# Kernel tuning notes

Measured on AMD Instinct MI355X. Metric: run time of the kernel, lower is better.

Reference implementation:

```python
import jax, jax.numpy as jnp
import numpy as np

B, N = 64, 8192
RW_APPROX_THRES = 0.6
L_CUTOFF = 100
EPS = 1e-12


def _skew(k):
    kx, ky, kz = k[..., 0], k[..., 1], k[..., 2]
    z = jnp.zeros_like(kx)
    return jnp.stack([
        jnp.stack([z, -kz, ky], -1),
        jnp.stack([kz, z, -kx], -1),
        jnp.stack([-ky, kx, z], -1)], -2)


def so3_exp(v):
    # v: [..., 3] rotation vector -> [..., 3, 3] rotation matrix (Rodrigues)
    theta = jnp.linalg.norm(v, axis=-1, keepdims=True)
    k = v / jnp.maximum(theta, 1e-12)
    K = _skew(k)
    s = jnp.sin(theta)[..., None]
    c = jnp.cos(theta)[..., None]
    I = jnp.eye(3, dtype=v.dtype)
    return I + s * K + (1.0 - c) * (K @ K)


def so3_log(r):
    # r: [..., 3, 3] rotation matrix -> [..., 3] rotation vector
    tr = r[..., 0, 0] + r[..., 1, 1] + r[..., 2, 2]
    cos = jnp.clip((tr - 1.0) * 0.5, -1.0 + 1e-7, 1.0 - 1e-7)
    theta = jnp.arccos(cos)  # [...]
    a = jnp.stack([
        r[..., 2, 1] - r[..., 1, 2],
        r[..., 0, 2] - r[..., 2, 0],
        r[..., 1, 0] - r[..., 0, 1]], axis=-1)  # [..., 3]
    scale = theta / (2.0 * jnp.sin(theta))
    return a * scale[..., None]


def igso3_grad_log_pdf(sigma, omega):
    # sigma: [B], omega: [B, N] angles in (0, pi)
    # f(w) = sum_l (2l+1) exp(-l(l+1) sigma^2 / 2) sin((l+1/2) w) / sin(w/2)
    l = jnp.arange(L_CUTOFF + 1, dtype=omega.dtype)          # [L]
    s2 = (sigma ** 2)[:, None, None]                          # [B,1,1]
    coef = (2.0 * l + 1.0) * jnp.exp(-l * (l + 1.0) * s2 / 2.0)  # [B,1,L]
    w = omega[..., None]                                      # [B,N,1]
    lh = l + 0.5
    sin_h = jnp.sin(w / 2.0)
    cos_h = jnp.cos(w / 2.0)
    sin_lw = jnp.sin(lh * w)                                  # [B,N,L]
    f = jnp.sum(coef * sin_lw / sin_h, axis=-1)               # [B,N]
    df = jnp.sum(coef * (lh * jnp.cos(lh * w) * sin_h - 0.5 * cos_h * sin_lw) / (sin_h ** 2), axis=-1)
    return df / (f + EPS)


def setup_inputs() -> dict:
    key = jax.random.key(0)
    k1, k2, k3, k4, k5 = jax.random.split(key, 5)
    ax1 = jax.random.normal(k1, (B, N, 3), dtype=jnp.float32)
    ax1 = ax1 / jnp.linalg.norm(ax1, axis=-1, keepdims=True)
    ang1 = jax.random.uniform(k2, (B, N, 1), minval=0.1, maxval=3.0, dtype=jnp.float32)
    r_t = so3_exp(ax1 * ang1)
    ax2 = jax.random.normal(k3, (B, N, 3), dtype=jnp.float32)
    ax2 = ax2 / jnp.linalg.norm(ax2, axis=-1, keepdims=True)
    ang2 = jax.random.uniform(k4, (B, N, 1), minval=0.1, maxval=3.0, dtype=jnp.float32)
    rh_0 = so3_exp(ax2 * ang2)
    sigma_t = jax.random.uniform(k5, (B,), minval=0.7, maxval=2.5, dtype=jnp.float32)
    return {"r_t": r_t, "rh_0": rh_0, "sigma_t": sigma_t}


def reference(r_t, rh_0, sigma_t):
    # RotationDiffuser.score with left=True
    r_z = jnp.einsum('bnij,bnkj->bnik', r_t, rh_0)  # r_t @ rh_0^T
    v_z = so3_log(r_z)                               # [B,N,3]
    rw_approx = -v_z / (sigma_t[:, None, None] ** 2)
    w = jnp.linalg.norm(v_z, axis=-1)                # [B,N]
    dlogf_dw = igso3_grad_log_pdf(sigma_t, w)        # [B,N]
    score = jnp.where(sigma_t[:, None, None] > RW_APPROX_THRES,
                      v_z * dlogf_dw[..., None] / (w[..., None] + EPS),
                      rw_approx)
    return score
```

## Files before the change

### kernel.cpp

```cpp
#include <hip/hip_runtime.h>
#include <math.h>


#define BD 256
#define LMAX 100

__device__ __forceinline__ float opq(float x) { __asm__("" : "+v"(x)); return x; }
__device__ __forceinline__ float MULF(float a, float b) { return opq(a * b); }
__device__ __forceinline__ float ADDF(float a, float b) { return opq(a + b); }
__device__ __forceinline__ float SUBF(float a, float b) { return opq(a - b); }
__device__ __forceinline__ float FMAF(float a, float b, float c) { return opq(__builtin_fmaf(a, b, c)); }
__device__ __forceinline__ float DOT3F(float a0, float b0, float a1, float b1,
                                       float a2, float b2) {
    return FMAF(a2, b2, FMAF(a1, b1, MULF(a0, b0)));
}

__device__ __forceinline__ double asin_p(double u) {
    double p = 0.00515311;
    p = __builtin_fma(p, u, 0.00574004);
    p = __builtin_fma(p, u, 0.0064472);
    p = __builtin_fma(p, u, 0.007312526);
    p = __builtin_fma(p, u, 0.008390335809616815);
    p = __builtin_fma(p, u, 0.009761609529194078);
    p = __builtin_fma(p, u, 0.011551800896139706);
    p = __builtin_fma(p, u, 0.01396484375);
    p = __builtin_fma(p, u, 0.017352764423076924);
    p = __builtin_fma(p, u, 0.022372159090909092);
    p = __builtin_fma(p, u, 0.030381944444444444);
    p = __builtin_fma(p, u, 0.044642857142857144);
    p = __builtin_fma(p, u, 0.075);
    p = __builtin_fma(p, u, 0.16666666666666666);
    p = __builtin_fma(p, u, 1.0);
    return p;
}
__device__ __forceinline__ double sin_p(double u) {
    double p = 2.8114572543455206e-15;
    p = __builtin_fma(p, u, -7.647163731819816e-13);
    p = __builtin_fma(p, u, 1.6059043836821613e-10);
    p = __builtin_fma(p, u, -2.505210838544172e-8);
    p = __builtin_fma(p, u, 2.7557319223985893e-6);
    p = __builtin_fma(p, u, -1.984126984126984e-4);
    p = __builtin_fma(p, u, 8.333333333333333e-3);
    p = __builtin_fma(p, u, -0.16666666666666666);
    p = __builtin_fma(p, u, 1.0);
    return p;
}
__device__ __forceinline__ double cos_p(double u) {
    double p = 4.779477332387385e-14;
    p = __builtin_fma(p, u, -1.1470745597729725e-11);
    p = __builtin_fma(p, u, 2.08767569878681e-9);
    p = __builtin_fma(p, u, -2.755731922398589e-7);
    p = __builtin_fma(p, u, 2.48015873015873e-5);
    p = __builtin_fma(p, u, -1.3888888888888889e-3);
    p = __builtin_fma(p, u, 0.041666666666666664);
    p = __builtin_fma(p, u, -0.5);
    p = __builtin_fma(p, u, 1.0);
    return p;
}
__device__ __forceinline__ double exp_d(double x) {
    double n = __builtin_rint(x * 1.4426950408889634);
    double r = __builtin_fma(-n, 6.93147180369123816490e-01, x);
    r = __builtin_fma(-n, 1.90821492927058770002e-10, r);
    double p = 2.08767569878681e-9;
    p = __builtin_fma(p, r, 2.505210838544172e-8);
    p = __builtin_fma(p, r, 2.755731922398589e-7);
    p = __builtin_fma(p, r, 2.48015873015873e-5);
    p = __builtin_fma(p, r, 1.984126984126984e-4);
    p = __builtin_fma(p, r, 1.3888888888888889e-3);
    p = __builtin_fma(p, r, 8.333333333333333e-3);
    p = __builtin_fma(p, r, 0.041666666666666664);
    p = __builtin_fma(p, r, 0.16666666666666666);
    p = __builtin_fma(p, r, 0.5);
    p = __builtin_fma(p, r, 1.0);
    p = __builtin_fma(p, r, 1.0);
    return p * exp2(n);
}

__global__ __launch_bounds__(BD) void rot_score_kernel(
    const float* __restrict__ rt, const float* __restrict__ rh,
    const float* __restrict__ sigma_t, float* __restrict__ out, int npts)
{
    __shared__ float  sA[BD * 9];
    __shared__ float  sB[BD * 9];
    __shared__ float  sCoef[LMAX + 1];
    __shared__ double sCoefL[LMAX + 1];

    const int tid = threadIdx.x;
    const int blocksPerB = npts / BD;
    const int b = blockIdx.x / blocksPerB;
    const size_t base = (size_t)blockIdx.x * BD;

    const float sigma = sigma_t[b];
    const float s2 = MULF(sigma, sigma);

    const float* gA = rt + base * 9;
    const float* gB = rh + base * 9;
#pragma unroll
    for (int k = 0; k < 9; ++k) {
        int i = tid + k * BD;
        sA[i] = gA[i];
        sB[i] = gB[i];
    }
    if (tid <= LMAX) {
        float lf = (float)tid;
        float t  = MULF(MULF(-lf, lf + 1.0f), s2);
        float arg = t * 0.5f;
        float e  = (float)exp_d((double)arg);
        float cf = MULF(2.0f * lf + 1.0f, e);
        sCoef[tid]  = cf;
        sCoefL[tid] = (double)cf * ((double)lf + 0.5);
    }
    __syncthreads();

    const int o = tid * 9;
    float a0 = sA[o+0], a1 = sA[o+1], a2 = sA[o+2];
    float a3 = sA[o+3], a4 = sA[o+4], a5 = sA[o+5];
    float a6 = sA[o+6], a7 = sA[o+7], a8 = sA[o+8];
    float b0 = sB[o+0], b1 = sB[o+1], b2 = sB[o+2];
    float b3 = sB[o+3], b4 = sB[o+4], b5 = sB[o+5];
    float b6 = sB[o+6], b7 = sB[o+7], b8 = sB[o+8];

    float m00 = DOT3F(a0,b0, a1,b1, a2,b2);
    float m11 = DOT3F(a3,b3, a4,b4, a5,b5);
    float m22 = DOT3F(a6,b6, a7,b7, a8,b8);
    float m01 = DOT3F(a0,b3, a1,b4, a2,b5);
    float m10 = DOT3F(a3,b0, a4,b1, a5,b2);
    float m02 = DOT3F(a0,b6, a1,b7, a2,b8);
    float m20 = DOT3F(a6,b0, a7,b1, a8,b2);
    float m12 = DOT3F(a3,b6, a4,b7, a5,b8);
    float m21 = DOT3F(a6,b3, a7,b4, a8,b5);

    float tr   = ADDF(ADDF(m00, m11), m22);
    float cosv = MULF(SUBF(tr, 1.0f), 0.5f);
    const float CLO = (float)(-1.0 + 1e-7);
    const float CHI = (float)( 1.0 - 1e-7);
    cosv = fminf(fmaxf(cosv, CLO), CHI);

    double xd = (double)cosv;
    double axd = fabs(xd);
    bool mid = (axd <= 0.5);
    double uedge = (1.0 - axd) * 0.5;
    double m = mid ? xd : sqrt(uedge);
    double asv = m * asin_p(m * m);
    double th_mid  = 1.5707963267948966 - asv;
    double th_edge = (xd > 0.0) ? (2.0 * asv)
                                : (3.141592653589793 - 2.0 * asv);
    double theta_d = mid ? th_mid : th_edge;
    float theta = (float)theta_d;

    double td = (double)theta;
    double e  = (td > 1.5707963267948966) ? (3.141592653589793 - td) : td;
    float st  = (float)(e * sin_p(e * e));

    float scale = (float)((double)theta / (double)(2.0f * st));
    float ax = SUBF(m21, m12);
    float ay = SUBF(m02, m20);
    float az = SUBF(m10, m01);
    float vx = MULF(ax, scale);
    float vy = MULF(ay, scale);
    float vz = MULF(az, scale);
    float ssum = ADDF(ADDF(MULF(vx,vx), MULF(vy,vy)), MULF(vz,vz));
    float w = (float)sqrt((double)ssum);

    double wd = (double)w;
    double h  = 0.5 * wd;
    double h2 = h * h;
    double shd = h * sin_p(h2);
    double chd = cos_p(h2);
    double swd = 2.0 * shd * chd;
    double cwd = 1.0 - 2.0 * shd * shd;

    double s = shd, c = chd;
    double S1 = 0.0, S2 = 0.0;
    for (int l = 0; l <= LMAX; ++l) {
        double cf = (double)sCoef[l];
        if (cf == 0.0) break;
        S1 = __builtin_fma(cf,        s, S1);
        S2 = __builtin_fma(sCoefL[l], c, S2);
        double ns = __builtin_fma(s, cwd,  c * swd);
        double nc = __builtin_fma(c, cwd, -(s * swd));
        s = ns; c = nc;
    }
    double f  = S1 / shd;
    double df = (S2 * shd - 0.5 * chd * S1) / (shd * shd);
    double g  = df / ((f + 1e-12) * (wd + 1e-12));

    float ox, oy, oz;
    if (sigma > 0.6f) {
        ox = (float)((double)vx * g);
        oy = (float)((double)vy * g);
        oz = (float)((double)vz * g);
    } else {
        ox = (float)((double)(-vx) / (double)s2);
        oy = (float)((double)(-vy) / (double)s2);
        oz = (float)((double)(-vz) / (double)s2);
    }

    __syncthreads();
    sA[tid * 3 + 0] = ox;
    sA[tid * 3 + 1] = oy;
    sA[tid * 3 + 2] = oz;
    __syncthreads();
    float* gO = out + base * 3;
#pragma unroll
    for (int k = 0; k < 3; ++k) {
        int i = tid + k * BD;
        gO[i] = sA[i];
    }
}

extern "C" void kernel_launch(void* const* d_in, const int* in_sizes, int n_in,
                              void* d_out, int out_size, void* d_ws, size_t ws_size,
                              hipStream_t stream) {
    const float* r_t     = (const float*)d_in[0];
    const float* rh_0    = (const float*)d_in[1];
    const float* sigma_t = (const float*)d_in[2];
    float* out = (float*)d_out;

    const int nB = in_sizes[2];
    const int n_elem = in_sizes[0] / 9;
    const int npts = n_elem / nB;
    const int grid = n_elem / BD;

    rot_score_kernel<<<grid, BD, 0, stream>>>(r_t, rh_0, sigma_t, out, npts);
}
```

Measured before the change: 84.72 us.

## Compute IGSO3 series in fp32 with sigma-based truncation and packed coefficients

Moves the l-series recurrence, the half-angle sin/cos polynomials and the final score arithmetic from double to float. The loop count is now derived analytically from sigma, replacing the per-iteration zero check. Coefficients are packed as float2 in shared memory, and exp2 is replaced by exponent bit construction. This removes the slow fp64 throughput on the dominant loop, at the risk of lower accuracy near small angles and in the f/df cancellation.

```diff
diff --git a/kernel.cpp b/kernel.cpp
--- a/kernel.cpp
+++ b/kernel.cpp
@@ -33,7 +33,7 @@
     p = __builtin_fma(p, u, 1.0);
     return p;
 }
-__device__ __forceinline__ double sin_p(double u) {
+__device__ __forceinline__ double sin_pd(double u) {
     double p = 2.8114572543455206e-15;
     p = __builtin_fma(p, u, -7.647163731819816e-13);
     p = __builtin_fma(p, u, 1.6059043836821613e-10);
@@ -45,19 +45,27 @@
     p = __builtin_fma(p, u, 1.0);
     return p;
 }
-__device__ __forceinline__ double cos_p(double u) {
-    double p = 4.779477332387385e-14;
-    p = __builtin_fma(p, u, -1.1470745597729725e-11);
-    p = __builtin_fma(p, u, 2.08767569878681e-9);
-    p = __builtin_fma(p, u, -2.755731922398589e-7);
-    p = __builtin_fma(p, u, 2.48015873015873e-5);
-    p = __builtin_fma(p, u, -1.3888888888888889e-3);
-    p = __builtin_fma(p, u, 0.041666666666666664);
-    p = __builtin_fma(p, u, -0.5);
-    p = __builtin_fma(p, u, 1.0);
+__device__ __forceinline__ float sin_pf(float u) {
+    float p = -2.5052108e-8f;
+    p = __builtin_fmaf(p, u, 2.75573192e-6f);
+    p = __builtin_fmaf(p, u, -1.98412698e-4f);
+    p = __builtin_fmaf(p, u, 8.33333333e-3f);
+    p = __builtin_fmaf(p, u, -0.166666667f);
+    p = __builtin_fmaf(p, u, 1.0f);
+    return p;
+}
+__device__ __forceinline__ float cos_pf(float u) {
+    float p = 2.08767570e-9f;
+    p = __builtin_fmaf(p, u, -2.75573192e-7f);
+    p = __builtin_fmaf(p, u, 2.48015873e-5f);
+    p = __builtin_fmaf(p, u, -1.38888889e-3f);
+    p = __builtin_fmaf(p, u, 4.16666667e-2f);
+    p = __builtin_fmaf(p, u, -0.5f);
+    p = __builtin_fmaf(p, u, 1.0f);
     return p;
 }
 __device__ __forceinline__ double exp_d(double x) {
+    if (x < -110.0) return 0.0;
     double n = __builtin_rint(x * 1.4426950408889634);
     double r = __builtin_fma(-n, 6.93147180369123816490e-01, x);
     r = __builtin_fma(-n, 1.90821492927058770002e-10, r);
@@ -73,7 +81,9 @@
     p = __builtin_fma(p, r, 0.5);
     p = __builtin_fma(p, r, 1.0);
     p = __builtin_fma(p, r, 1.0);
-    return p * exp2(n);
+    long long ni = (long long)n;
+    double p2 = __longlong_as_double((1023ll + ni) << 52);
+    return p * p2;
 }
 
 __global__ __launch_bounds__(BD) void rot_score_kernel(
@@ -82,8 +92,7 @@
 {
     __shared__ float  sA[BD * 9];
     __shared__ float  sB[BD * 9];
-    __shared__ float  sCoef[LMAX + 1];
-    __shared__ double sCoefL[LMAX + 1];
+    __shared__ float2 sC[LMAX + 1];
 
     const int tid = threadIdx.x;
     const int blocksPerB = npts / BD;
@@ -107,8 +116,7 @@
         float arg = t * 0.5f;
         float e  = (float)exp_d((double)arg);
         float cf = MULF(2.0f * lf + 1.0f, e);
-        sCoef[tid]  = cf;
-        sCoefL[tid] = (double)cf * ((double)lf + 0.5);
+        sC[tid] = make_float2(cf, cf * (lf + 0.5f));
     }
     __syncthreads();
 
@@ -150,8 +158,7 @@
 
     double td = (double)theta;
     double e  = (td > 1.5707963267948966) ? (3.141592653589793 - td) : td;
-    float st  = (float)(e * sin_p(e * e));
-
+    float st  = (float)(e * sin_pd(e * e));
     float scale = (float)((double)theta / (double)(2.0f * st));
     float ax = SUBF(m21, m12);
     float ay = SUBF(m02, m20);
@@ -162,38 +169,37 @@
     float ssum = ADDF(ADDF(MULF(vx,vx), MULF(vy,vy)), MULF(vz,vz));
     float w = (float)sqrt((double)ssum);
 
-    double wd = (double)w;
-    double h  = 0.5 * wd;
-    double h2 = h * h;
-    double shd = h * sin_p(h2);
-    double chd = cos_p(h2);
-    double swd = 2.0 * shd * chd;
-    double cwd = 1.0 - 2.0 * shd * shd;
-
-    double s = shd, c = chd;
-    double S1 = 0.0, S2 = 0.0;
-    for (int l = 0; l <= LMAX; ++l) {
-        double cf = (double)sCoef[l];
-        if (cf == 0.0) break;
-        S1 = __builtin_fma(cf,        s, S1);
-        S2 = __builtin_fma(sCoefL[l], c, S2);
-        double ns = __builtin_fma(s, cwd,  c * swd);
-        double nc = __builtin_fma(c, cwd, -(s * swd));
+    float wh = 0.5f * w;
+    float u  = wh * wh;
+    float sh = wh * sin_pf(u);
+    float ch = cos_pf(u);
+    float sw = 2.0f * sh * ch;
+    float cw = __builtin_fmaf(-2.0f * sh, sh, 1.0f);
+
+    int nl = (int)ceilf((-1.0f + sqrtf(1.0f + 880.0f / s2)) * 0.5f) + 1;
+    if (nl > LMAX + 1) nl = LMAX + 1;
+
+    float s = sh, c = ch;
+    float S1 = 0.0f, S2 = 0.0f;
+#pragma unroll 2
+    for (int l = 0; l < nl; ++l) {
+        float2 cc = sC[l];
+        S1 = __builtin_fmaf(cc.x, s, S1);
+        S2 = __builtin_fmaf(cc.y, c, S2);
+        float ns = __builtin_fmaf(s, cw,  c * sw);
+        float nc = __builtin_fmaf(c, cw, -(s * sw));
         s = ns; c = nc;
     }
-    double f  = S1 / shd;
-    double df = (S2 * shd - 0.5 * chd * S1) / (shd * shd);
-    double g  = df / ((f + 1e-12) * (wd + 1e-12));
+    float num = __builtin_fmaf(S2, sh, -(0.5f * ch * S1));
+    float den = __builtin_fmaf(sh, S1, 1e-12f * sh * sh) * (w + 1e-12f);
+    float gf  = num / den;
 
     float ox, oy, oz;
     if (sigma > 0.6f) {
-        ox = (float)((double)vx * g);
-        oy = (float)((double)vy * g);
-        oz = (float)((double)vz * g);
+        ox = vx * gf; oy = vy * gf; oz = vz * gf;
     } else {
-        ox = (float)((double)(-vx) / (double)s2);
-        oy = (float)((double)(-vy) / (double)s2);
-        oz = (float)((double)(-vz) / (double)s2);
+        float gi = -1.0f / s2;
+        ox = vx * gi; oy = vy * gi; oz = vz * gi;
     }
 
     __syncthreads();
```

After: 82.00 us. 1.03x faster.
